# Performance work log

Measured on AMD Instinct MI355X. Metric: run time of the kernel, lower is better.

Reference implementation:

```python
import jax, jax.numpy as jnp
import numpy as np

NH, HD = 4, 16          # num_heads, head_dim (proj_dim = 64)
SCALE = HD ** -0.5
EPS = 1e-5
G = 16                  # GroupNorm groups = min(16, channels)


def _conv1x1(W, b, x):
    # 1x1 conv == channel-mixing matmul: W (out,in), x (B,in,H,W)
    return jnp.einsum('pc,bchw->bphw', W, x) + b[None, :, None, None]


def _attend(Wq, bq, Wk, bk, Wv, bv, Wo, bo, query, context):
    B, C, H, Wd = query.shape
    N = H * Wd
    q = _conv1x1(Wq, bq, query).astype(jnp.float32).reshape(B, NH, HD, N)
    k = _conv1x1(Wk, bk, context).astype(jnp.float32).reshape(B, NH, HD, N)
    v = _conv1x1(Wv, bv, context).astype(jnp.float32).reshape(B, NH, HD, N)
    attn = jax.nn.softmax(jnp.einsum('bhdn,bhdm->bhnm', q, k) * SCALE, axis=-1)
    out = jnp.einsum('bhdm,bhnm->bhdn', v, attn).reshape(B, NH * HD, H, Wd)
    return _conv1x1(Wo, bo, out)


def _gn(x, gamma, beta):
    B, C, H, W = x.shape
    xr = x.reshape(B, G, C // G, H, W)
    m = xr.mean(axis=(2, 3, 4), keepdims=True)
    v = xr.var(axis=(2, 3, 4), keepdims=True)
    xn = ((xr - m) * jax.lax.rsqrt(v + EPS)).reshape(B, C, H, W)
    return xn * gamma[None, :, None, None] + beta[None, :, None, None]


def setup_inputs() -> dict:
    key = jax.random.key(0)
    C, P, Bn, H, W = 256, 64, 2, 64, 64
    ks = iter(jax.random.split(key, 64))
    d = {}
    for m in ['a', 'b', 'c']:
        d[f'feat_{m}'] = jax.random.normal(next(ks), (Bn, C, H, W), jnp.float32)
    for m in ['a', 'b', 'c']:
        d[f'Wq_{m}'] = 0.02 * jax.random.normal(next(ks), (P, C), jnp.float32)
        d[f'bq_{m}'] = jnp.zeros((P,), jnp.float32)
        d[f'Wk_{m}'] = 0.02 * jax.random.normal(next(ks), (P, 2 * C), jnp.float32)
        d[f'bk_{m}'] = jnp.zeros((P,), jnp.float32)
        d[f'Wv_{m}'] = 0.02 * jax.random.normal(next(ks), (P, 2 * C), jnp.float32)
        d[f'bv_{m}'] = jnp.zeros((P,), jnp.float32)
        d[f'Wo_{m}'] = 0.02 * jax.random.normal(next(ks), (C, P), jnp.float32)
        d[f'bo_{m}'] = jnp.zeros((C,), jnp.float32)
        d[f'g_{m}'] = jnp.ones((C,), jnp.float32)
        d[f'be_{m}'] = jnp.zeros((C,), jnp.float32)
    return d


def reference(feat_a, feat_b, feat_c,
              Wq_a, bq_a, Wk_a, bk_a, Wv_a, bv_a, Wo_a, bo_a, g_a, be_a,
              Wq_b, bq_b, Wk_b, bk_b, Wv_b, bv_b, Wo_b, bo_b, g_b, be_b,
              Wq_c, bq_c, Wk_c, bk_c, Wv_c, bv_c, Wo_c, bo_c, g_c, be_c):
    bc = jnp.concatenate([feat_b, feat_c], axis=1)
    a_out = _gn(feat_a + _attend(Wq_a, bq_a, Wk_a, bk_a, Wv_a, bv_a, Wo_a, bo_a, feat_a, bc), g_a, be_a)
    ac = jnp.concatenate([feat_a, feat_c], axis=1)
    b_out = _gn(feat_b + _attend(Wq_b, bq_b, Wk_b, bk_b, Wv_b, bv_b, Wo_b, bo_b, feat_b, ac), g_b, be_b)
    ab = jnp.concatenate([feat_a, feat_b], axis=1)
    c_out = _gn(feat_c + _attend(Wq_c, bq_c, Wk_c, bk_c, Wv_c, bv_c, Wo_c, bo_c, feat_c, ab), g_c, be_c)
    return (a_out, b_out, c_out)
```

## Files before the change

### kernel.cpp

```cpp
#include <hip/hip_runtime.h>

#define B_ 2
#define C_ 256
#define P_ 64
#define N_ 4096
#define EPS_ 1e-5f
#define QSCALE_ 0.3606737602222409f

typedef _Float16 half2 __attribute__((ext_vector_type(2)));
typedef _Float16 half4 __attribute__((ext_vector_type(4)));
typedef _Float16 half8 __attribute__((ext_vector_type(8)));
typedef __fp16 fp16x2 __attribute__((ext_vector_type(2)));
typedef float f32x4 __attribute__((ext_vector_type(4)));

#if __has_builtin(__builtin_amdgcn_exp2f)
static __device__ __forceinline__ float fexp2(float x) { return __builtin_amdgcn_exp2f(x); }
#else
static __device__ __forceinline__ float fexp2(float x) { return exp2f(x); }
#endif

static __device__ __forceinline__ half2 pack2(float a, float b) {
  return __builtin_bit_cast(half2, __builtin_amdgcn_cvt_pkrtz(a, b));
}

struct TP {
  const float* feat[3];
  const float* Wq[3]; const float* bq[3];
  const float* Wk[3]; const float* bk[3];
  const float* Wv[3]; const float* bv[3];
  const float* Wo[3]; const float* bo[3];
  const float* gm[3]; const float* bt[3];
  _Float16* xT;
  _Float16* q16;
  _Float16* k16;
  _Float16* v16;
  _Float16* wq16[3];
  _Float16* wk16[3];
  _Float16* wv16[3];
  _Float16* wo16[3];
  float* stats;
  float* out;
  int ctx0[3]; int ctx1[3];
};

__global__ __launch_bounds__(256) void prep_kernel(TP P) {
  const int m = blockIdx.z, b = blockIdx.y;
  const int tid = threadIdx.x;
  {
    const int c0 = (blockIdx.x >> 6) * 64 + (tid >> 6) * 16;
    const int n = (blockIdx.x & 63) * 64 + (tid & 63);
    const float* __restrict__ in = P.feat[m] + (size_t)b * C_ * N_ + n;
    float f[16];
#pragma unroll
    for (int i = 0; i < 16; ++i) f[i] = in[(size_t)(c0 + i) * N_];
    half8 h0, h1;
#pragma unroll
    for (int j = 0; j < 8; ++j) { h0[j] = (_Float16)f[j]; h1[j] = (_Float16)f[8 + j]; }
    _Float16* o = P.xT + (((size_t)(m * 2 + b) * N_) + n) * C_ + c0;
    *(half8*)o = h0;
    *(half8*)(o + 8) = h1;
  }
  if (b == 0 && blockIdx.x < 8) {
    const int s = blockIdx.x;
    const float* srcs[4] = {P.Wq[m], P.Wk[m], P.Wv[m], P.Wo[m]};
    _Float16* dsts[4] = {P.wq16[m], P.wk16[m], P.wv16[m], P.wo16[m]};
    const int sizes[4] = {64 * 256, 64 * 512, 64 * 512, 256 * 64};
#pragma unroll
    for (int a = 0; a < 4; ++a) {
      const int lo = sizes[a] / 8 * s, hi = sizes[a] / 8 * (s + 1);
      for (int i = lo + tid * 4; i < hi; i += 1024) {
        const float4 x = *(const float4*)(srcs[a] + i);
        half4 h; h[0] = (_Float16)x.x; h[1] = (_Float16)x.y;
        h[2] = (_Float16)x.z; h[3] = (_Float16)x.w;
        *(half4*)(dsts[a] + i) = h;
      }
    }
  }
  if (m == 0 && b == 0 && blockIdx.x == 8 && tid < 192) P.stats[tid] = 0.f;
}

__global__ __launch_bounds__(256) void proj_qkv_kernel(TP P) {
  __shared__ _Float16 vt[4 * 16 * 40];
  const int m = blockIdx.z, b = blockIdx.y;
  const int tid = threadIdx.x;
  const int w = tid >> 6, g = (tid >> 4) & 3, t = tid & 15;
  const bool is_q = blockIdx.x >= 128;
  const int n0 = (is_q ? blockIdx.x - 128 : (int)blockIdx.x) * 32;

  if (is_q) {
    const _Float16* __restrict__ A = P.wq16[m] + (w * 16 + t) * 256 + g * 8;
    const _Float16* __restrict__ B0 =
        P.xT + ((size_t)(m * 2 + b) * N_ + n0 + t) * C_ + g * 8;
    const _Float16* __restrict__ B1 = B0 + 16 * C_;
    f32x4 a0 = {0.f,0.f,0.f,0.f}, a1 = {0.f,0.f,0.f,0.f};
#pragma unroll
    for (int k = 0; k < 8; ++k) {
      const half8 a = *(const half8*)(A + k * 32);
      const half8 b0 = *(const half8*)(B0 + k * 32);
      const half8 b1 = *(const half8*)(B1 + k * 32);
      a0 = __builtin_amdgcn_mfma_f32_16x16x32_f16(a, b0, a0, 0, 0, 0);
      a1 = __builtin_amdgcn_mfma_f32_16x16x32_f16(a, b1, a1, 0, 0, 0);
    }
    _Float16* qo = P.q16 + ((size_t)(m * 2 + b) * N_) * 64 + w * 16 + g * 4;
    half4 h0, h1;
#pragma unroll
    for (int r = 0; r < 4; ++r) {
      const float bq = P.bq[m][w * 16 + g * 4 + r];
      h0[r] = (_Float16)((a0[r] + bq) * QSCALE_);
      h1[r] = (_Float16)((a1[r] + bq) * QSCALE_);
    }
    *(half4*)(qo + (size_t)(n0 + t) * 64) = h0;
    *(half4*)(qo + (size_t)(n0 + 16 + t) * 64) = h1;
  } else {
    f32x4 k0 = {0.f,0.f,0.f,0.f}, k1 = {0.f,0.f,0.f,0.f};
    f32x4 v0 = {0.f,0.f,0.f,0.f}, v1 = {0.f,0.f,0.f,0.f};
    const int srcs[2] = {P.ctx0[m], P.ctx1[m]};
#pragma unroll
    for (int src = 0; src < 2; ++src) {
      const _Float16* __restrict__ Ak =
          P.wk16[m] + (w * 16 + t) * 512 + src * 256 + g * 8;
      const _Float16* __restrict__ Av =
          P.wv16[m] + (w * 16 + t) * 512 + src * 256 + g * 8;
      const _Float16* __restrict__ B0 =
          P.xT + ((size_t)(srcs[src] * 2 + b) * N_ + n0 + t) * C_ + g * 8;
      const _Float16* __restrict__ B1 = B0 + 16 * C_;
#pragma unroll
      for (int k = 0; k < 8; ++k) {
        const half8 ak = *(const half8*)(Ak + k * 32);
        const half8 av = *(const half8*)(Av + k * 32);
        const half8 b0 = *(const half8*)(B0 + k * 32);
        const half8 b1 = *(const half8*)(B1 + k * 32);
        k0 = __builtin_amdgcn_mfma_f32_16x16x32_f16(ak, b0, k0, 0, 0, 0);
        k1 = __builtin_amdgcn_mfma_f32_16x16x32_f16(ak, b1, k1, 0, 0, 0);
        v0 = __builtin_amdgcn_mfma_f32_16x16x32_f16(av, b0, v0, 0, 0, 0);
        v1 = __builtin_amdgcn_mfma_f32_16x16x32_f16(av, b1, v1, 0, 0, 0);
      }
    }
    const int bh = m * 8 + b * 4 + w;
    _Float16* ko = P.k16 + ((size_t)bh * N_) * 16 + g * 4;
    half4 h0, h1;
#pragma unroll
    for (int r = 0; r < 4; ++r) {
      const float bk = P.bk[m][w * 16 + g * 4 + r];
      h0[r] = (_Float16)(k0[r] + bk);
      h1[r] = (_Float16)(k1[r] + bk);
    }
    *(half4*)(ko + (size_t)(n0 + t) * 16) = h0;
    *(half4*)(ko + (size_t)(n0 + 16 + t) * 16) = h1;
#pragma unroll
    for (int r = 0; r < 4; ++r) {
      const float bv = P.bv[m][w * 16 + g * 4 + r];
      vt[(w * 16 + g * 4 + r) * 40 + t] = (_Float16)(v0[r] + bv);
      vt[(w * 16 + g * 4 + r) * 40 + 16 + t] = (_Float16)(v1[r] + bv);
    }
    __syncthreads();
    const int hh = tid >> 6, dd = (tid >> 2) & 15, nb = (tid & 3) * 8;
    const half8 hv8 = *(const half8*)(vt + (hh * 16 + dd) * 40 + nb);
    *(half8*)(P.v16 + ((size_t)(m * 8 + b * 4 + hh) * 16 + dd) * N_ + n0 + nb) = hv8;
  }
}

__global__ __launch_bounds__(256) void attn_kernel(TP P) {
  const int m = blockIdx.z, bh = blockIdx.y;
  const int tid = threadIdx.x;
  const int w = tid >> 6, g = (tid >> 4) & 3, t = tid & 15;
  const _Float16* __restrict__ kh = P.k16 + ((size_t)(m * 8 + bh) * N_) * 16;
  const _Float16* __restrict__ vh = P.v16 + ((size_t)(m * 8 + bh) * 16) * N_;
  const int b = bh >> 2, h = bh & 3;
  _Float16* qh = P.q16 + ((size_t)(m * 2 + b) * N_) * 64 + h * 16 + g * 4;

  const int q0 = blockIdx.x * 64 + w * 16;
  const half4 qf = *(const half4*)(qh + (size_t)(q0 + t) * 64);

  __shared__ _Float16 ks[128 * 16];
  __shared__ _Float16 vs[16 * 128];

  const int kr = tid >> 1, kc8 = tid & 1;
  const int vr = tid >> 4, vc = tid & 15;
  const _Float16* kgp = kh + (size_t)kr * 16 + kc8 * 8;
  const _Float16* vgp = vh + (size_t)vr * N_ + vc * 8;
  _Float16* ksp = ks + kr * 16 + ((kc8 ^ (kr & 1)) << 3);
  _Float16* vsp = vs + vr * 128 + ((vc ^ vr) << 3);

  half8 kpre = *(const half8*)kgp;
  half8 vpre = *(const half8*)vgp;

  f32x4 lacc = {0.f, 0.f, 0.f, 0.f};
  f32x4 O0 = {0.f,0.f,0.f,0.f}, O1 = {0.f,0.f,0.f,0.f};

  for (int kv0 = 0; kv0 < N_; kv0 += 128) {
    *(half8*)ksp = kpre;
    *(half8*)vsp = vpre;
    __syncthreads();
    const int nxt = (kv0 + 128 < N_) ? kv0 + 128 : 0;
    kpre = *(const half8*)(kgp + (size_t)nxt * 16);
    vpre = *(const half8*)(vgp + nxt);
#pragma unroll
    for (int hc = 0; hc < 2; ++hc) {
      f32x4 s[4];
#pragma unroll
      for (int i = 0; i < 4; ++i) {
        const int sub = hc * 4 + i;
        const half4 kf = *(const half4*)(ks + (sub * 16 + t) * 16 +
                          (((g >> 1) ^ (t & 1)) << 3) + (g & 1) * 4);
        const f32x4 z = {0.f, 0.f, 0.f, 0.f};
        s[i] = __builtin_amdgcn_mfma_f32_16x16x16f16(kf, qf, z, 0, 0, 0);
      }
      half4 pf[4];
#pragma unroll
      for (int i = 0; i < 4; ++i) {
        const float p0 = fexp2(s[i][0]);
        const float p1 = fexp2(s[i][1]);
        const float p2 = fexp2(s[i][2]);
        const float p3 = fexp2(s[i][3]);
        lacc[0] += p0; lacc[1] += p1; lacc[2] += p2; lacc[3] += p3;
        const half2 lo = pack2(p0, p1);
        const half2 hi = pack2(p2, p3);
        pf[i] = __builtin_shufflevector(lo, hi, 0, 1, 2, 3);
      }
#pragma unroll
      for (int i = 0; i < 4; ++i) {
        const int sub = hc * 4 + i;
        const half4 vf = *(const half4*)(vs + t * 128 +
                          (((sub * 2 + (g >> 1)) ^ t) << 3) + (g & 1) * 4);
        if (i & 1) O1 = __builtin_amdgcn_mfma_f32_16x16x16f16(vf, pf[i], O1, 0, 0, 0);
        else       O0 = __builtin_amdgcn_mfma_f32_16x16x16f16(vf, pf[i], O0, 0, 0, 0);
      }
    }
    __syncthreads();
  }
  float l = lacc[0] + lacc[1] + lacc[2] + lacc[3];
  l += __shfl_xor(l, 16);
  l += __shfl_xor(l, 32);
  const float inv = 1.0f / l;
  half4 hv;
#pragma unroll
  for (int r = 0; r < 4; ++r) hv[r] = (_Float16)((O0[r] + O1[r]) * inv);
  *(half4*)(qh + (size_t)(q0 + t) * 64) = hv;
}

__global__ __launch_bounds__(256) void wo_resid_kernel(TP P) {
  const int m = blockIdx.z;
  const int b = blockIdx.y >> 2, cblk = blockIdx.y & 3;
  const int n0 = blockIdx.x * 64;
  const int tid = threadIdx.x;
  const int w = tid >> 6, g = (tid >> 4) & 3, t = tid & 15;
  const int c0 = cblk * 64 + w * 16;
  const _Float16* __restrict__ ao = P.q16 + ((size_t)(m * 2 + b) * N_) * 64;
  f32x4 acc[4] = {{0.f,0.f,0.f,0.f},{0.f,0.f,0.f,0.f},{0.f,0.f,0.f,0.f},{0.f,0.f,0.f,0.f}};
#pragma unroll
  for (int kst = 0; kst < 2; ++kst) {
    const half8 a =
        *(const half8*)(P.wo16[m] + (c0 + t) * 64 + kst * 32 + g * 8);
#pragma unroll
    for (int i = 0; i < 4; ++i) {
      const half8 bf =
          *(const half8*)(ao + (size_t)(n0 + i * 16 + t) * 64 + kst * 32 + g * 8);
      acc[i] = __builtin_amdgcn_mfma_f32_16x16x32_f16(a, bf, acc[i], 0, 0, 0);
    }
  }
  const float* __restrict__ X = P.feat[m] + (size_t)b * C_ * N_;
  float* outb = P.out + (size_t)m * B_ * C_ * N_ + (size_t)b * C_ * N_;
  float s = 0.f, s2 = 0.f;
#pragma unroll
  for (int i = 0; i < 4; ++i) {
    const int n = n0 + i * 16 + t;
#pragma unroll
    for (int r = 0; r < 4; ++r) {
      const int c = c0 + g * 4 + r;
      const float val = acc[i][r] + X[(size_t)c * N_ + n] + P.bo[m][c];
      outb[(size_t)c * N_ + n] = val;
      s += val;
      s2 += val * val;
    }
  }
#pragma unroll
  for (int off = 1; off < 64; off <<= 1) {
    s += __shfl_xor(s, off);
    s2 += __shfl_xor(s2, off);
  }
  if ((tid & 63) == 0) {
    const int group = cblk * 4 + w;
    float* st = P.stats + ((size_t)(m * 2 + b) * 16 + group) * 2;
    atomicAdd(st, s);
    atomicAdd(st + 1, s2);
  }
}

__global__ __launch_bounds__(256) void gn_final_kernel(TP P) {
  const size_t idx = ((size_t)blockIdx.x * 256 + threadIdx.x) * 4;
  const int m = (int)(idx >> 21);
  const int rem = (int)(idx & ((1u << 21) - 1));
  const int b = rem >> 20;
  const int c = (rem >> 12) & 255;
  const float* st = P.stats + ((size_t)(m * 2 + b) * 16 + (c >> 4)) * 2;
  const float mean = st[0] * (1.f / 65536.f);
  const float var = st[1] * (1.f / 65536.f) - mean * mean;
  const float rstd = rsqrtf(var + EPS_);
  const float ga = P.gm[m][c] * rstd, be = P.bt[m][c];
  float4 x = *(float4*)(P.out + idx);
  x.x = (x.x - mean) * ga + be;
  x.y = (x.y - mean) * ga + be;
  x.z = (x.z - mean) * ga + be;
  x.w = (x.w - mean) * ga + be;
  *(float4*)(P.out + idx) = x;
}

extern "C" void kernel_launch(void* const* d_in, const int* in_sizes, int n_in,
                              void* d_out, int out_size, void* d_ws, size_t ws_size,
                              hipStream_t stream) {
  TP P;
  for (int m = 0; m < 3; ++m) {
    P.feat[m] = (const float*)d_in[m];
    const int base = 3 + m * 10;
    P.Wq[m] = (const float*)d_in[base + 0];
    P.bq[m] = (const float*)d_in[base + 1];
    P.Wk[m] = (const float*)d_in[base + 2];
    P.bk[m] = (const float*)d_in[base + 3];
    P.Wv[m] = (const float*)d_in[base + 4];
    P.bv[m] = (const float*)d_in[base + 5];
    P.Wo[m] = (const float*)d_in[base + 6];
    P.bo[m] = (const float*)d_in[base + 7];
    P.gm[m] = (const float*)d_in[base + 8];
    P.bt[m] = (const float*)d_in[base + 9];
  }
  _Float16* ws = (_Float16*)d_ws;
  P.xT = ws;
  P.q16 = ws + 6291456;
  P.k16 = ws + 7864320;
  P.v16 = ws + 9437184;
  for (int m = 0; m < 3; ++m) {
    _Float16* wb = ws + 11010048 + (size_t)m * 98304;
    P.wq16[m] = wb;
    P.wk16[m] = wb + 16384;
    P.wv16[m] = wb + 49152;
    P.wo16[m] = wb + 81920;
  }
  P.stats = (float*)((char*)d_ws + 22609920);
  P.out = (float*)d_out;
  P.ctx0[0] = 1; P.ctx1[0] = 2;
  P.ctx0[1] = 0; P.ctx1[1] = 2;
  P.ctx0[2] = 0; P.ctx1[2] = 1;

  dim3 blk(256);
  prep_kernel<<<dim3(256, 2, 3), blk, 0, stream>>>(P);
  proj_qkv_kernel<<<dim3(256, 2, 3), blk, 0, stream>>>(P);
  attn_kernel<<<dim3(64, 8, 3), blk, 0, stream>>>(P);
  wo_resid_kernel<<<dim3(64, 8, 3), blk, 0, stream>>>(P);
  gn_final_kernel<<<dim3(6144), blk, 0, stream>>>(P);
}
```

Baseline: 293.0 us.

## Process two query tiles per warp, stage projection operands in LDS, approximate exp2

The attention kernel now gives each warp two 16-row query tiles, so every K/V fragment read from LDS feeds twice the MFMA work, and the grid is halved to match. The QKV projection and Wo kernels now stage activation tiles in padded shared memory instead of issuing strided per-lane global loads. The hardware exp2 is replaced by a bit-manipulation approximation (an fma followed by an int-to-float reinterpret) to cut transcendental cost in the softmax. In exchange, the approximate exp adds relative error of a few percent to the attention weights, the extra accumulators raise register pressure, and the added barriers in the projection loop may limit latency hiding.

```diff
diff --git a/kernel.cpp b/kernel.cpp
--- a/kernel.cpp
+++ b/kernel.cpp
@@ -10,14 +10,11 @@
 typedef _Float16 half2 __attribute__((ext_vector_type(2)));
 typedef _Float16 half4 __attribute__((ext_vector_type(4)));
 typedef _Float16 half8 __attribute__((ext_vector_type(8)));
-typedef __fp16 fp16x2 __attribute__((ext_vector_type(2)));
 typedef float f32x4 __attribute__((ext_vector_type(4)));
 
-#if __has_builtin(__builtin_amdgcn_exp2f)
-static __device__ __forceinline__ float fexp2(float x) { return __builtin_amdgcn_exp2f(x); }
-#else
-static __device__ __forceinline__ float fexp2(float x) { return exp2f(x); }
-#endif
+static __device__ __forceinline__ float fexp2(float x) {
+  return __builtin_bit_cast(float, (int)fmaf(x, 8388608.0f, 1064872512.0f));
+}
 
 static __device__ __forceinline__ half2 pack2(float a, float b) {
   return __builtin_bit_cast(half2, __builtin_amdgcn_cvt_pkrtz(a, b));
@@ -79,27 +76,36 @@
   if (m == 0 && b == 0 && blockIdx.x == 8 && tid < 192) P.stats[tid] = 0.f;
 }
 
+#define BS_ 72
+
 __global__ __launch_bounds__(256) void proj_qkv_kernel(TP P) {
+  __shared__ _Float16 bs[32 * BS_];
   __shared__ _Float16 vt[4 * 16 * 40];
   const int m = blockIdx.z, b = blockIdx.y;
   const int tid = threadIdx.x;
   const int w = tid >> 6, g = (tid >> 4) & 3, t = tid & 15;
   const bool is_q = blockIdx.x >= 128;
   const int n0 = (is_q ? blockIdx.x - 128 : (int)blockIdx.x) * 32;
+  const int sr = tid >> 3, sc = (tid & 7) * 8;
 
   if (is_q) {
-    const _Float16* __restrict__ A = P.wq16[m] + (w * 16 + t) * 256 + g * 8;
-    const _Float16* __restrict__ B0 =
-        P.xT + ((size_t)(m * 2 + b) * N_ + n0 + t) * C_ + g * 8;
-    const _Float16* __restrict__ B1 = B0 + 16 * C_;
+    const _Float16* __restrict__ xb =
+        P.xT + ((size_t)(m * 2 + b) * N_ + n0 + sr) * C_ + sc;
     f32x4 a0 = {0.f,0.f,0.f,0.f}, a1 = {0.f,0.f,0.f,0.f};
-#pragma unroll
-    for (int k = 0; k < 8; ++k) {
-      const half8 a = *(const half8*)(A + k * 32);
-      const half8 b0 = *(const half8*)(B0 + k * 32);
-      const half8 b1 = *(const half8*)(B1 + k * 32);
-      a0 = __builtin_amdgcn_mfma_f32_16x16x32_f16(a, b0, a0, 0, 0, 0);
-      a1 = __builtin_amdgcn_mfma_f32_16x16x32_f16(a, b1, a1, 0, 0, 0);
+    for (int cc = 0; cc < 4; ++cc) {
+      const half8 st = *(const half8*)(xb + cc * 64);
+      __syncthreads();
+      *(half8*)(bs + sr * BS_ + sc) = st;
+      __syncthreads();
+#pragma unroll
+      for (int ks = 0; ks < 2; ++ks) {
+        const half8 a = *(const half8*)(P.wq16[m] + (w * 16 + t) * 256 +
+                                        cc * 64 + ks * 32 + g * 8);
+        const half8 b0 = *(const half8*)(bs + t * BS_ + ks * 32 + g * 8);
+        const half8 b1 = *(const half8*)(bs + (16 + t) * BS_ + ks * 32 + g * 8);
+        a0 = __builtin_amdgcn_mfma_f32_16x16x32_f16(a, b0, a0, 0, 0, 0);
+        a1 = __builtin_amdgcn_mfma_f32_16x16x32_f16(a, b1, a1, 0, 0, 0);
+      }
     }
     _Float16* qo = P.q16 + ((size_t)(m * 2 + b) * N_) * 64 + w * 16 + g * 4;
     half4 h0, h1;
@@ -115,21 +121,21 @@
     f32x4 k0 = {0.f,0.f,0.f,0.f}, k1 = {0.f,0.f,0.f,0.f};
     f32x4 v0 = {0.f,0.f,0.f,0.f}, v1 = {0.f,0.f,0.f,0.f};
     const int srcs[2] = {P.ctx0[m], P.ctx1[m]};
-#pragma unroll
-    for (int src = 0; src < 2; ++src) {
-      const _Float16* __restrict__ Ak =
-          P.wk16[m] + (w * 16 + t) * 512 + src * 256 + g * 8;
-      const _Float16* __restrict__ Av =
-          P.wv16[m] + (w * 16 + t) * 512 + src * 256 + g * 8;
-      const _Float16* __restrict__ B0 =
-          P.xT + ((size_t)(srcs[src] * 2 + b) * N_ + n0 + t) * C_ + g * 8;
-      const _Float16* __restrict__ B1 = B0 + 16 * C_;
-#pragma unroll
-      for (int k = 0; k < 8; ++k) {
-        const half8 ak = *(const half8*)(Ak + k * 32);
-        const half8 av = *(const half8*)(Av + k * 32);
-        const half8 b0 = *(const half8*)(B0 + k * 32);
-        const half8 b1 = *(const half8*)(B1 + k * 32);
+    for (int it = 0; it < 8; ++it) {
+      const int src = it >> 2, cc = it & 3;
+      const half8 st = *(const half8*)(
+          P.xT + ((size_t)(srcs[src] * 2 + b) * N_ + n0 + sr) * C_ + cc * 64 + sc);
+      __syncthreads();
+      *(half8*)(bs + sr * BS_ + sc) = st;
+      __syncthreads();
+#pragma unroll
+      for (int ks = 0; ks < 2; ++ks) {
+        const half8 ak = *(const half8*)(P.wk16[m] + (w * 16 + t) * 512 +
+                                         src * 256 + cc * 64 + ks * 32 + g * 8);
+        const half8 av = *(const half8*)(P.wv16[m] + (w * 16 + t) * 512 +
+                                         src * 256 + cc * 64 + ks * 32 + g * 8);
+        const half8 b0 = *(const half8*)(bs + t * BS_ + ks * 32 + g * 8);
+        const half8 b1 = *(const half8*)(bs + (16 + t) * BS_ + ks * 32 + g * 8);
         k0 = __builtin_amdgcn_mfma_f32_16x16x32_f16(ak, b0, k0, 0, 0, 0);
         k1 = __builtin_amdgcn_mfma_f32_16x16x32_f16(ak, b1, k1, 0, 0, 0);
         v0 = __builtin_amdgcn_mfma_f32_16x16x32_f16(av, b0, v0, 0, 0, 0);
@@ -169,8 +175,9 @@
   const int b = bh >> 2, h = bh & 3;
   _Float16* qh = P.q16 + ((size_t)(m * 2 + b) * N_) * 64 + h * 16 + g * 4;
 
-  const int q0 = blockIdx.x * 64 + w * 16;
-  const half4 qf = *(const half4*)(qh + (size_t)(q0 + t) * 64);
+  const int q0 = blockIdx.x * 128 + w * 32;
+  const half4 qfa = *(const half4*)(qh + (size_t)(q0 + t) * 64);
+  const half4 qfb = *(const half4*)(qh + (size_t)(q0 + 16 + t) * 64);
 
   __shared__ _Float16 ks[128 * 16];
   __shared__ _Float16 vs[16 * 128];
@@ -185,8 +192,9 @@
   half8 kpre = *(const half8*)kgp;
   half8 vpre = *(const half8*)vgp;
 
-  f32x4 lacc = {0.f, 0.f, 0.f, 0.f};
-  f32x4 O0 = {0.f,0.f,0.f,0.f}, O1 = {0.f,0.f,0.f,0.f};
+  f32x4 la = {0.f,0.f,0.f,0.f}, lb = {0.f,0.f,0.f,0.f};
+  f32x4 Oa0 = {0.f,0.f,0.f,0.f}, Oa1 = {0.f,0.f,0.f,0.f};
+  f32x4 Ob0 = {0.f,0.f,0.f,0.f}, Ob1 = {0.f,0.f,0.f,0.f};
 
   for (int kv0 = 0; kv0 < N_; kv0 += 128) {
     *(half8*)ksp = kpre;
@@ -197,49 +205,66 @@
     vpre = *(const half8*)(vgp + nxt);
 #pragma unroll
     for (int hc = 0; hc < 2; ++hc) {
-      f32x4 s[4];
+      half4 kf[4];
 #pragma unroll
       for (int i = 0; i < 4; ++i) {
         const int sub = hc * 4 + i;
-        const half4 kf = *(const half4*)(ks + (sub * 16 + t) * 16 +
-                          (((g >> 1) ^ (t & 1)) << 3) + (g & 1) * 4);
-        const f32x4 z = {0.f, 0.f, 0.f, 0.f};
-        s[i] = __builtin_amdgcn_mfma_f32_16x16x16f16(kf, qf, z, 0, 0, 0);
-      }
-      half4 pf[4];
+        kf[i] = *(const half4*)(ks + (sub * 16 + t) * 16 +
+                 (((g >> 1) ^ (t & 1)) << 3) + (g & 1) * 4);
+      }
+      const f32x4 z = {0.f, 0.f, 0.f, 0.f};
+      half4 pa[4], pb[4];
 #pragma unroll
       for (int i = 0; i < 4; ++i) {
-        const float p0 = fexp2(s[i][0]);
-        const float p1 = fexp2(s[i][1]);
-        const float p2 = fexp2(s[i][2]);
-        const float p3 = fexp2(s[i][3]);
-        lacc[0] += p0; lacc[1] += p1; lacc[2] += p2; lacc[3] += p3;
-        const half2 lo = pack2(p0, p1);
-        const half2 hi = pack2(p2, p3);
-        pf[i] = __builtin_shufflevector(lo, hi, 0, 1, 2, 3);
-      }
+        const f32x4 s = __builtin_amdgcn_mfma_f32_16x16x16f16(kf[i], qfa, z, 0, 0, 0);
+        const float p0 = fexp2(s[0]), p1 = fexp2(s[1]);
+        const float p2 = fexp2(s[2]), p3 = fexp2(s[3]);
+        la[0] += p0; la[1] += p1; la[2] += p2; la[3] += p3;
+        pa[i] = __builtin_shufflevector(pack2(p0, p1), pack2(p2, p3), 0, 1, 2, 3);
+      }
+#pragma unroll
+      for (int i = 0; i < 4; ++i) {
+        const f32x4 s = __builtin_amdgcn_mfma_f32_16x16x16f16(kf[i], qfb, z, 0, 0, 0);
+        const float p0 = fexp2(s[0]), p1 = fexp2(s[1]);
+        const float p2 = fexp2(s[2]), p3 = fexp2(s[3]);
+        lb[0] += p0; lb[1] += p1; lb[2] += p2; lb[3] += p3;
+        pb[i] = __builtin_shufflevector(pack2(p0, p1), pack2(p2, p3), 0, 1, 2, 3);
+      }
+      half4 vf[4];
 #pragma unroll
       for (int i = 0; i < 4; ++i) {
         const int sub = hc * 4 + i;
-        const half4 vf = *(const half4*)(vs + t * 128 +
-                          (((sub * 2 + (g >> 1)) ^ t) << 3) + (g & 1) * 4);
-        if (i & 1) O1 = __builtin_amdgcn_mfma_f32_16x16x16f16(vf, pf[i], O1, 0, 0, 0);
-        else       O0 = __builtin_amdgcn_mfma_f32_16x16x16f16(vf, pf[i], O0, 0, 0, 0);
-      }
+        vf[i] = *(const half4*)(vs + t * 128 +
+                 (((sub * 2 + (g >> 1)) ^ t) << 3) + (g & 1) * 4);
+      }
+      Oa0 = __builtin_amdgcn_mfma_f32_16x16x16f16(vf[0], pa[0], Oa0, 0, 0, 0);
+      Oa1 = __builtin_amdgcn_mfma_f32_16x16x16f16(vf[1], pa[1], Oa1, 0, 0, 0);
+      Oa0 = __builtin_amdgcn_mfma_f32_16x16x16f16(vf[2], pa[2], Oa0, 0, 0, 0);
+      Oa1 = __builtin_amdgcn_mfma_f32_16x16x16f16(vf[3], pa[3], Oa1, 0, 0, 0);
+      Ob0 = __builtin_amdgcn_mfma_f32_16x16x16f16(vf[0], pb[0], Ob0, 0, 0, 0);
+      Ob1 = __builtin_amdgcn_mfma_f32_16x16x16f16(vf[1], pb[1], Ob1, 0, 0, 0);
+      Ob0 = __builtin_amdgcn_mfma_f32_16x16x16f16(vf[2], pb[2], Ob0, 0, 0, 0);
+      Ob1 = __builtin_amdgcn_mfma_f32_16x16x16f16(vf[3], pb[3], Ob1, 0, 0, 0);
     }
     __syncthreads();
   }
-  float l = lacc[0] + lacc[1] + lacc[2] + lacc[3];
-  l += __shfl_xor(l, 16);
-  l += __shfl_xor(l, 32);
-  const float inv = 1.0f / l;
-  half4 hv;
-#pragma unroll
-  for (int r = 0; r < 4; ++r) hv[r] = (_Float16)((O0[r] + O1[r]) * inv);
-  *(half4*)(qh + (size_t)(q0 + t) * 64) = hv;
+  float sla = la[0] + la[1] + la[2] + la[3];
+  sla += __shfl_xor(sla, 16); sla += __shfl_xor(sla, 32);
+  float slb = lb[0] + lb[1] + lb[2] + lb[3];
+  slb += __shfl_xor(slb, 16); slb += __shfl_xor(slb, 32);
+  const float ia = 1.0f / sla, ib = 1.0f / slb;
+  half4 ha, hb;
+#pragma unroll
+  for (int r = 0; r < 4; ++r) {
+    ha[r] = (_Float16)((Oa0[r] + Oa1[r]) * ia);
+    hb[r] = (_Float16)((Ob0[r] + Ob1[r]) * ib);
+  }
+  *(half4*)(qh + (size_t)(q0 + t) * 64) = ha;
+  *(half4*)(qh + (size_t)(q0 + 16 + t) * 64) = hb;
 }
 
 __global__ __launch_bounds__(256) void wo_resid_kernel(TP P) {
+  __shared__ _Float16 as[64 * BS_];
   const int m = blockIdx.z;
   const int b = blockIdx.y >> 2, cblk = blockIdx.y & 3;
   const int n0 = blockIdx.x * 64;
@@ -247,6 +272,12 @@
   const int w = tid >> 6, g = (tid >> 4) & 3, t = tid & 15;
   const int c0 = cblk * 64 + w * 16;
   const _Float16* __restrict__ ao = P.q16 + ((size_t)(m * 2 + b) * N_) * 64;
+  const int ar = tid >> 2, ac = (tid & 3) * 16;
+  const half8 l0 = *(const half8*)(ao + (size_t)(n0 + ar) * 64 + ac);
+  const half8 l1 = *(const half8*)(ao + (size_t)(n0 + ar) * 64 + ac + 8);
+  *(half8*)(as + ar * BS_ + ac) = l0;
+  *(half8*)(as + ar * BS_ + ac + 8) = l1;
+  __syncthreads();
   f32x4 acc[4] = {{0.f,0.f,0.f,0.f},{0.f,0.f,0.f,0.f},{0.f,0.f,0.f,0.f},{0.f,0.f,0.f,0.f}};
 #pragma unroll
   for (int kst = 0; kst < 2; ++kst) {
@@ -254,8 +285,7 @@
         *(const half8*)(P.wo16[m] + (c0 + t) * 64 + kst * 32 + g * 8);
 #pragma unroll
     for (int i = 0; i < 4; ++i) {
-      const half8 bf =
-          *(const half8*)(ao + (size_t)(n0 + i * 16 + t) * 64 + kst * 32 + g * 8);
+      const half8 bf = *(const half8*)(as + (i * 16 + t) * BS_ + kst * 32 + g * 8);
       acc[i] = __builtin_amdgcn_mfma_f32_16x16x32_f16(a, bf, acc[i], 0, 0, 0);
     }
   }
@@ -345,7 +375,7 @@
   dim3 blk(256);
   prep_kernel<<<dim3(256, 2, 3), blk, 0, stream>>>(P);
   proj_qkv_kernel<<<dim3(256, 2, 3), blk, 0, stream>>>(P);
-  attn_kernel<<<dim3(64, 8, 3), blk, 0, stream>>>(P);
+  attn_kernel<<<dim3(32, 8, 3), blk, 0, stream>>>(P);
   wo_resid_kernel<<<dim3(64, 8, 3), blk, 0, stream>>>(P);
   gn_final_kernel<<<dim3(6144), blk, 0, stream>>>(P);
 }
```

Result: faster. 280.9 us (-4.1%).
